# Kernel tuning notes

Measured on AMD Instinct MI355X. Metric: run time of the kernel, lower is better.

## Reference

```python
import jax, jax.numpy as jnp
import numpy as np

N_NODES = 20000
N_EDGES = 320000
N_GRAPHS = 64
D = 128  # node_dim


def _gat_conv(h, W, al, ar, b, src, dst, n, res=None, act=None):
    # DGL GATConv: fc -> per-head attn logits -> leaky_relu -> edge softmax per dst -> scatter-add
    H, Dh = al.shape
    feat = (h @ W).reshape(n, H, Dh)                      # [N,H,D]
    el = jnp.einsum('nhd,hd->nh', feat, al)               # [N,H]
    er = jnp.einsum('nhd,hd->nh', feat, ar)               # [N,H]
    e = jax.nn.leaky_relu(el[src] + er[dst], 0.2)         # [E,H]
    m = jax.ops.segment_max(e, dst, num_segments=n)       # [N,H]
    m = jnp.where(jnp.isfinite(m), m, 0.0)
    a = jnp.exp(e - m[dst])                               # [E,H]
    den = jax.ops.segment_sum(a, dst, num_segments=n)     # [N,H]
    a = a / jnp.maximum(den, 1e-9)[dst]
    out = jax.ops.segment_sum(a[:, :, None] * feat[src], dst, num_segments=n)  # [N,H,D]
    if res is not None:
        out = out + res
    out = out + b.reshape(1, H, Dh)
    return act(out) if act is not None else out


def setup_inputs() -> dict:
    key = jax.random.key(0)
    ks = jax.random.split(key, 20)
    s = 0.05
    inp = {
        'h': jax.random.normal(ks[0], (N_NODES, D), jnp.float32),
        'he': jax.random.normal(ks[1], (N_EDGES, 64), jnp.float32),
        'src': jax.random.randint(ks[2], (N_EDGES,), 0, N_NODES),
        'dst': jax.random.randint(ks[3], (N_EDGES,), 0, N_NODES),
        'graph_id': jnp.sort(jax.random.randint(ks[4], (N_NODES,), 0, N_GRAPHS)),
        # layer 0: in=D, heads=4, out=D
        'W0': jax.random.normal(ks[5], (D, 4 * D), jnp.float32) * s,
        'al0': jax.random.normal(ks[6], (4, D), jnp.float32) * s,
        'ar0': jax.random.normal(ks[7], (4, D), jnp.float32) * s,
        'b0': jnp.zeros((4 * D,), jnp.float32),
        # layer 1: in=4D, heads=4, out=D, residual (identity since 4D==4*D)
        'W1': jax.random.normal(ks[8], (4 * D, 4 * D), jnp.float32) * s,
        'al1': jax.random.normal(ks[9], (4, D), jnp.float32) * s,
        'ar1': jax.random.normal(ks[10], (4, D), jnp.float32) * s,
        'b1': jnp.zeros((4 * D,), jnp.float32),
        # layer 2: in=4D, heads=6, out=D, residual via res_fc (4D -> 6D)
        'W2': jax.random.normal(ks[11], (4 * D, 6 * D), jnp.float32) * s,
        'al2': jax.random.normal(ks[12], (6, D), jnp.float32) * s,
        'ar2': jax.random.normal(ks[13], (6, D), jnp.float32) * s,
        'b2': jnp.zeros((6 * D,), jnp.float32),
        'resW2': jax.random.normal(ks[14], (4 * D, 6 * D), jnp.float32) * s,
        # final MLP (1 layer): Linear(D, D)
        'Wm': jax.random.normal(ks[15], (D, D), jnp.float32) * s,
        'bm': jnp.zeros((D,), jnp.float32),
    }
    return inp


def reference(h, he, src, dst, graph_id, W0, al0, ar0, b0, W1, al1, ar1, b1,
              W2, al2, ar2, b2, resW2, Wm, bm):
    n = h.shape[0]
    elu = jax.nn.elu
    # layer 0 (no residual, elu), flatten heads
    x = _gat_conv(h, W0, al0, ar0, b0, src, dst, n, res=None, act=elu)
    x = x.reshape(n, -1)  # [N, 4D]
    # layer 1 (identity residual, elu), flatten heads
    res1 = x.reshape(n, 4, D)
    x2 = _gat_conv(x, W1, al1, ar1, b1, src, dst, n, res=res1, act=elu)
    x2 = x2.reshape(n, -1)  # [N, 4D]
    # layer 2 (linear residual, no activation), mean over heads
    res2 = (x2 @ resW2).reshape(n, 6, D)
    x3 = _gat_conv(x2, W2, al2, ar2, b2, src, dst, n, res=res2, act=None)
    local_feat = x3.mean(axis=1)  # [N, D]
    # avg pooling per graph + linear
    sums = jax.ops.segment_sum(local_feat, graph_id, num_segments=N_GRAPHS)
    cnts = jax.ops.segment_sum(jnp.ones((n,), local_feat.dtype), graph_id, num_segments=N_GRAPHS)
    pooled = sums / jnp.maximum(cnts, 1.0)[:, None]  # [G, D]
    global_feat = pooled @ Wm + bm
    return (local_feat, global_feat)
```

## Files before the change

### kernel.cpp

```cpp
#include <hip/hip_runtime.h>
#include <math.h>


typedef _Float16 f16;
typedef __attribute__((ext_vector_type(8))) _Float16 half8;
typedef __attribute__((ext_vector_type(4))) _Float16 half4;
typedef __attribute__((ext_vector_type(4))) float float4v;

union U16 { unsigned short u; _Float16 h; };

#define M_PAD 20096
#define CHSTRIDE ((size_t)M_PAD * 64)

__device__ inline void gload_lds16(const void* g, void* l) {
    __builtin_amdgcn_global_load_lds((const __attribute__((address_space(1))) unsigned*)g,
                                     (__attribute__((address_space(3))) unsigned*)l,
                                     16, 0, 0);
}


__global__ __launch_bounds__(256) void deg_kernel(const int* __restrict__ dst,
                                                  int* __restrict__ deg, int E) {
    int e = blockIdx.x * 256 + threadIdx.x;
    if (e < E) atomicAdd(&deg[dst[e]], 1);
}

__global__ __launch_bounds__(1024) void scan_kernel(const int* __restrict__ deg,
                                                    int* __restrict__ row_off,
                                                    const int* __restrict__ gid,
                                                    int* __restrict__ gstart, int n) {
    __shared__ int sums[1024];
    int t = threadIdx.x;
    if (t <= 64) {
        int g = t, lo = 0, hi = n;
        while (lo < hi) {
            int mid = (lo + hi) >> 1;
            if (gid[mid] < g) lo = mid + 1; else hi = mid;
        }
        gstart[g] = lo;
    }
    int CH = (n + 1023) >> 10;
    int base = t * CH;
    int s = 0;
    for (int i = 0; i < CH; ++i) { int idx = base + i; if (idx < n) s += deg[idx]; }
    sums[t] = s;
    __syncthreads();
    for (int off = 1; off < 1024; off <<= 1) {
        int v = (t >= off) ? sums[t - off] : 0;
        __syncthreads();
        sums[t] += v;
        __syncthreads();
    }
    int run = (t == 0) ? 0 : sums[t - 1];
    for (int i = 0; i < CH; ++i) {
        int idx = base + i;
        if (idx < n) { row_off[idx] = run; run += deg[idx]; }
    }
    if (t == 1023) row_off[n] = run;
}

__global__ __launch_bounds__(256) void fill_kernel(const int* __restrict__ src,
                                                   const int* __restrict__ dst,
                                                   const int* __restrict__ row_off,
                                                   int* __restrict__ fill,
                                                   int* __restrict__ csr_src, int E) {
    int e = blockIdx.x * 256 + threadIdx.x;
    if (e < E) {
        int d = dst[e];
        int pos = row_off[d] + atomicAdd(&fill[d], 1);
        csr_src[pos] = src[e];
    }
}


__global__ __launch_bounds__(256) void prep_kernel(
        const float* __restrict__ h, f16* __restrict__ h16,
        f16* __restrict__ x1, f16* __restrict__ x2,
        const float* __restrict__ W0, f16* __restrict__ Wt0,
        const float* __restrict__ W1, f16* __restrict__ Wt1,
        const float* __restrict__ W2, const float* __restrict__ resW2,
        f16* __restrict__ Wt2cat,
        int* __restrict__ deg2, int n) {
    __shared__ float tile[32][33];
    int b = blockIdx.x;
    int t = threadIdx.x;
    if (b < 2512) {
        long i = ((long)b * 256 + t) * 4;
        long nv = (long)n * 128;
        float4 v = make_float4(0.f, 0.f, 0.f, 0.f);
        if (i < nv) v = *(const float4*)&h[i];
        half4 o; o[0] = (f16)v.x; o[1] = (f16)v.y; o[2] = (f16)v.z; o[3] = (f16)v.w;
        *(half4*)&h16[i] = o;
        return;
    }
    b -= 2512;
    if (b < 48) {
        int idx = (b * 256 + t) * 4;
        int total = (M_PAD - n) * 512;
        if (idx < total) {
            half4 z; z[0] = (f16)0.f; z[1] = (f16)0.f; z[2] = (f16)0.f; z[3] = (f16)0.f;
            *(half4*)&x1[(size_t)n * 512 + idx] = z;
            *(half4*)&x2[(size_t)n * 512 + idx] = z;
        }
        return;
    }
    b -= 48;
    {
        const float* W = nullptr; f16* Wt = nullptr;
        int K = 0, N = 0, bx = 0, by = 0;
        bool dotr = false;
        if (b < 64)        { W = W0; Wt = Wt0;    K = 128; N = 512; bx = b & 15;  by = b >> 4; dotr = true; }
        else if (b < 320)  { int r = b - 64;  W = W1; Wt = Wt1;    K = 512; N = 512; bx = r & 15;  by = r >> 4; dotr = true; }
        else if (b < 704)  { int r = b - 320; W = W2; Wt = Wt2cat; K = 512; N = 768; bx = r % 24;  by = r / 24; dotr = true; }
        if (dotr) {
            int tx = t & 31, ty = t >> 5;
            int n0 = bx * 32, k0 = by * 32;
#pragma unroll
            for (int i = 0; i < 32; i += 8)
                tile[ty + i][tx] = W[(size_t)(k0 + ty + i) * N + n0 + tx];
            __syncthreads();
#pragma unroll
            for (int i = 0; i < 32; i += 8)
                Wt[(size_t)(n0 + ty + i) * K + k0 + tx] = (f16)tile[tx][ty + i];
            return;
        }
    }
    b -= 704;
    if (b < 256) {
        int idx = b * 256 + t;
        int d = idx >> 9;
        int k = idx & 511;
        float s = 0.f;
#pragma unroll
        for (int hh = 0; hh < 6; ++hh) s += resW2[(size_t)k * 768 + hh * 128 + d];
        Wt2cat[(size_t)(768 + d) * 512 + k] = (f16)(s * (1.f / 6.f));
        return;
    }
    b -= 256;
    {
        int idx = (b * 256 + t) * 4;
        if (idx < 2 * n) *(int4*)&deg2[idx] = make_int4(0, 0, 0, 0);
    }
}


#define STAGE(buf, k0) do {                                   \
    f16* a_ = As + (buf) * 2048 + t * 8;                      \
    f16* b_ = Bs + (buf) * 4096 + t * 8;                      \
    gload_lds16(ag0 + (k0), a_);                              \
    gload_lds16(bg0 + (k0), b_);                              \
    gload_lds16(bg1 + (k0), b_ + 2048);                       \
} while (0)

__global__ __launch_bounds__(256) void gemm16_kernel(const f16* __restrict__ A,
                                                     const f16* __restrict__ Bt,
                                                     f16* __restrict__ Cc,
                                                     f16* __restrict__ Cr,
                                                     const float* __restrict__ al,
                                                     const float* __restrict__ ar,
                                                     float* __restrict__ el8,
                                                     float* __restrict__ er8,
                                                     int N, int K, int nchunk,
                                                     int nheads, int nvalid) {
    __shared__ f16 As[2 * 64 * 32];
    __shared__ f16 Bs[2 * 128 * 32];
    __shared__ float elds[2][2][64];
    int t = threadIdx.x;
    int w = t >> 6;
    int l = t & 63;

    int gx = gridDim.x;
    int nwg = gx * gridDim.y;
    int wg = blockIdx.y * gx + blockIdx.x;
    int qq = nwg >> 3, rr = nwg & 7;
    int xcd = wg & 7, idx = wg >> 3;
    int swz = (xcd < rr ? xcd * (qq + 1) : rr * (qq + 1) + (xcd - rr) * qq) + idx;
    int bxi = swz % gx;
    int byi = swz / gx;

    size_t bm = (size_t)byi * 64;
    int bn = bxi * 128;
    int wm = (w & 1) * 32;
    int wn = (w >> 1) * 64;

    int srow = t >> 2;
    int sq = (t & 3) ^ ((srow >> 1) & 3);
    const f16* ag0 = A + (bm + srow) * K + sq * 8;
    const f16* bg0 = Bt + (size_t)(bn + srow) * K + sq * 8;
    const f16* bg1 = Bt + (size_t)(bn + 64 + srow) * K + sq * 8;

    float4v acc[2][4];
#pragma unroll
    for (int i = 0; i < 2; ++i)
#pragma unroll
        for (int j = 0; j < 4; ++j) acc[i][j] = (float4v)(0.f);

    int ml = l & 15, q = l >> 4;
    int sslot = (q ^ ((ml >> 1) & 3)) * 8;
    int apoff = (wm + ml) * 32 + sslot;
    int bpoff = (wn + ml) * 32 + sslot;

    STAGE(0, 0);
    __syncthreads();
    int cur = 0;
    for (int k0 = 0; k0 < K; k0 += 32) {
        if (k0 + 32 < K) STAGE(cur ^ 1, k0 + 32);
        const f16* ap = As + cur * 2048 + apoff;
        const f16* bp = Bs + cur * 4096 + bpoff;
        half8 af[2], bf[4];
#pragma unroll
        for (int mt = 0; mt < 2; ++mt) af[mt] = *(const half8*)(ap + mt * 16 * 32);
#pragma unroll
        for (int nt = 0; nt < 4; ++nt) bf[nt] = *(const half8*)(bp + nt * 16 * 32);
#pragma unroll
        for (int mt = 0; mt < 2; ++mt)
#pragma unroll
            for (int nt = 0; nt < 4; ++nt)
                acc[mt][nt] = __builtin_amdgcn_mfma_f32_16x16x32_f16(bf[nt], af[mt],
                                                                     acc[mt][nt], 0, 0, 0);
        __syncthreads();
        cur ^= 1;
    }
#pragma unroll
    for (int mt = 0; mt < 2; ++mt) {
        size_t row = bm + wm + mt * 16 + ml;
#pragma unroll
        for (int nt = 0; nt < 4; ++nt) {
            half4 hv;
#pragma unroll
            for (int r = 0; r < 4; ++r) hv[r] = (f16)acc[mt][nt][r];
            int col = bn + wn + nt * 16 + q * 4;
            if (col < nchunk) {
                *(half4*)&Cc[(size_t)(col >> 6) * CHSTRIDE + row * 64 + (col & 63)] = hv;
            } else {
                *(half4*)&Cr[row * (size_t)(N - nchunk) + (col - nchunk)] = hv;
            }
        }
    }
    if (al != nullptr && bn < nheads * 128) {
        int hh = bn >> 7;
        float4 a4[4], r4[4];
#pragma unroll
        for (int nt = 0; nt < 4; ++nt) {
            int ci = hh * 128 + wn + nt * 16 + q * 4;
            a4[nt] = *(const float4*)&al[ci];
            r4[nt] = *(const float4*)&ar[ci];
        }
        int wnidx = wn >> 6;
#pragma unroll
        for (int mt = 0; mt < 2; ++mt) {
            float ep = 0.f, rp = 0.f;
#pragma unroll
            for (int nt = 0; nt < 4; ++nt) {
                ep += acc[mt][nt][0] * a4[nt].x + acc[mt][nt][1] * a4[nt].y
                    + acc[mt][nt][2] * a4[nt].z + acc[mt][nt][3] * a4[nt].w;
                rp += acc[mt][nt][0] * r4[nt].x + acc[mt][nt][1] * r4[nt].y
                    + acc[mt][nt][2] * r4[nt].z + acc[mt][nt][3] * r4[nt].w;
            }
            ep += __shfl_xor(ep, 16, 64); ep += __shfl_xor(ep, 32, 64);
            rp += __shfl_xor(rp, 16, 64); rp += __shfl_xor(rp, 32, 64);
            if (q == 0) {
                elds[0][wnidx][wm + mt * 16 + ml] = ep;
                elds[1][wnidx][wm + mt * 16 + ml] = rp;
            }
        }
        __syncthreads();
        if (((t >> 6) & 1) == 0) {
            int row = t & 63, which = t >> 7;
            long gv = (long)bm + row;
            if (gv < nvalid) {
                float vs = elds[which][0][row] + elds[which][1][row];
                if (which == 0) el8[gv * 8 + hh] = vs;
                else            er8[gv * 8 + hh] = vs;
            }
        }
    }
}


__global__ __launch_bounds__(256, 8) void edge_weight_kernel(
        const float* __restrict__ el8, const float* __restrict__ er8,
        const int* __restrict__ row_off, const int* __restrict__ csr_src,
        int* __restrict__ wp, float* __restrict__ inv8,
        int H, int n, int E) {
    int wid = threadIdx.x >> 6, lane = threadIdx.x & 63;
    int c2 = lane >> 4;
    int sl = lane & 15;
    int v = blockIdx.x * 16 + wid * 4 + c2;
    if (v >= n) return;
    float era[6];
    {
        float4 a = *(const float4*)&er8[(size_t)v * 8];
        float2 b = *(const float2*)&er8[(size_t)v * 8 + 4];
        era[0] = a.x; era[1] = a.y; era[2] = a.z; era[3] = a.w;
        era[4] = b.x; era[5] = b.y;
    }
    int beg = row_off[v], end = row_off[v + 1];
    float lsum[6] = {0.f, 0.f, 0.f, 0.f, 0.f, 0.f};
    for (int pos = beg; pos < end; pos += 16) {
        int cnt = min(16, end - pos);
        int s_l = (sl < cnt) ? csr_src[pos + sl] : 0;
        float4 a = *(const float4*)&el8[(size_t)s_l * 8];
        float2 bq = *(const float2*)&el8[(size_t)s_l * 8 + 4];
        float ee[6] = {a.x, a.y, a.z, a.w, bq.x, bq.y};
#pragma unroll
        for (int h = 0; h < 6; ++h) {
            if (h < H) {
                float lg = ee[h] + era[h];
                lg = (lg >= 0.f) ? lg : 0.2f * lg;
                float wv = __expf(lg);
                if (sl >= cnt) wv = 0.f;
                lsum[h] += wv;
                if (sl < cnt) {
                    U16 uu; uu.h = (f16)wv;
                    wp[(size_t)h * E + pos + sl] = s_l | ((int)uu.u << 16);
                }
            }
        }
    }
#pragma unroll
    for (int h = 0; h < 6; ++h)
#pragma unroll
        for (int off = 8; off >= 1; off >>= 1)
            lsum[h] += __shfl_xor(lsum[h], off, 64);
    if (sl == 0) {
#pragma unroll
        for (int h = 0; h < 6; ++h)
            if (h < H) inv8[(size_t)v * 8 + h] = 1.f / fmaxf(lsum[h], 1e-9f);
    }
}


__device__ __forceinline__ void agg_chunk_body(
        const f16* __restrict__ fc, const int* __restrict__ wp,
        const float* __restrict__ inv8, int head,
        const int* __restrict__ row_off,
        const f16* __restrict__ res, const float* __restrict__ bias,
        f16* __restrict__ out16, float* __restrict__ out32,
        int n, int width, int act, int chunk,
        int wave_id, int wavestride, int lane) {
    int c = lane >> 3;
    int j = lane & 7;
    int coff = j * 8;
    int cb = chunk * 64 + coff;
    float4 bv0 = *(const float4*)&bias[cb];
    float4 bv1 = *(const float4*)&bias[cb + 4];
    int clbase = lane & 56;

    for (int v0 = wave_id * 8; v0 < n; v0 += wavestride * 8) {
        int v = v0 + c;
        bool valid = (v < n);
        int beg = 0, end = 0;
        if (valid) { beg = row_off[v]; end = row_off[v + 1]; }
        int rounds = end - beg;
        rounds = max(rounds, __shfl_xor(rounds, 8, 64));
        rounds = max(rounds, __shfl_xor(rounds, 16, 64));
        rounds = max(rounds, __shfl_xor(rounds, 32, 64));
        float acc[8] = {0.f, 0.f, 0.f, 0.f, 0.f, 0.f, 0.f, 0.f};
        int pidx = beg + j;
        int pk = (pidx < end) ? wp[pidx] : 0;
        for (int base = 0; base < rounds; base += 8) {
            int pn = beg + base + 8 + j;
            int pk_nxt = (pn < end) ? wp[pn] : 0;
#pragma unroll
            for (int hg = 0; hg < 2; ++hg) {
                int cb4 = clbase + hg * 4;
                int p0 = __shfl(pk, cb4 + 0, 64);
                int p1 = __shfl(pk, cb4 + 1, 64);
                int p2 = __shfl(pk, cb4 + 2, 64);
                int p3 = __shfl(pk, cb4 + 3, 64);
                half8 f0 = *(const half8*)&fc[(size_t)(p0 & 0xFFFF) * 64 + coff];
                half8 f1 = *(const half8*)&fc[(size_t)(p1 & 0xFFFF) * 64 + coff];
                half8 f2 = *(const half8*)&fc[(size_t)(p2 & 0xFFFF) * 64 + coff];
                half8 f3 = *(const half8*)&fc[(size_t)(p3 & 0xFFFF) * 64 + coff];
                U16 u0; u0.u = (unsigned short)((unsigned)p0 >> 16); float w0 = (float)u0.h;
                U16 u1; u1.u = (unsigned short)((unsigned)p1 >> 16); float w1 = (float)u1.h;
                U16 u2; u2.u = (unsigned short)((unsigned)p2 >> 16); float w2 = (float)u2.h;
                U16 u3; u3.u = (unsigned short)((unsigned)p3 >> 16); float w3 = (float)u3.h;
#pragma unroll
                for (int k = 0; k < 8; ++k) acc[k] += w0 * (float)f0[k];
#pragma unroll
                for (int k = 0; k < 8; ++k) acc[k] += w1 * (float)f1[k];
#pragma unroll
                for (int k = 0; k < 8; ++k) acc[k] += w2 * (float)f2[k];
#pragma unroll
                for (int k = 0; k < 8; ++k) acc[k] += w3 * (float)f3[k];
            }
            pk = pk_nxt;
        }
        if (valid) {
            float inv = inv8[(size_t)v * 8 + head];
            float ox[8];
#pragma unroll
            for (int k = 0; k < 8; ++k) ox[k] = acc[k] * inv;
            size_t base = (size_t)v * width + cb;
            if (res) {
                half8 rr = *(const half8*)&res[base];
#pragma unroll
                for (int k = 0; k < 8; ++k) ox[k] += (float)rr[k];
            }
            ox[0] += bv0.x; ox[1] += bv0.y; ox[2] += bv0.z; ox[3] += bv0.w;
            ox[4] += bv1.x; ox[5] += bv1.y; ox[6] += bv1.z; ox[7] += bv1.w;
            if (act) {
#pragma unroll
                for (int k = 0; k < 8; ++k)
                    ox[k] = (ox[k] > 0.f) ? ox[k] : expm1f(ox[k]);
            }
            if (out16) {
                half8 o;
#pragma unroll
                for (int k = 0; k < 8; ++k) o[k] = (f16)ox[k];
                *(half8*)&out16[base] = o;
            } else {
                *(float4*)&out32[base]     = make_float4(ox[0], ox[1], ox[2], ox[3]);
                *(float4*)&out32[base + 4] = make_float4(ox[4], ox[5], ox[6], ox[7]);
            }
        }
    }
}

__global__ __launch_bounds__(256, 6) void agg_chunk_kernel(
        const f16* __restrict__ featc, const int* __restrict__ wp,
        const float* __restrict__ inv8,
        const int* __restrict__ row_off,
        const f16* __restrict__ res, const float* __restrict__ bias,
        f16* __restrict__ out16, float* __restrict__ out32,
        int n, int nchunks, int width, int E, int act) {
    int wid = threadIdx.x >> 6, lane = threadIdx.x & 63;
    int b = blockIdx.x;
    {
        int chunk = b & 7;
        agg_chunk_body(featc + (size_t)chunk * CHSTRIDE, wp + (size_t)(chunk >> 1) * E,
                       inv8, chunk >> 1, row_off, res, bias, out16, out32,
                       n, width, act, chunk, (b >> 3) * 4 + wid, 1024, lane);
    }
    if (nchunks > 8) {
        int chunk = 8 + (b & 3);
        if (chunk < nchunks)
            agg_chunk_body(featc + (size_t)chunk * CHSTRIDE, wp + (size_t)(chunk >> 1) * E,
                           inv8, chunk >> 1, row_off, res, bias, out16, out32,
                           n, width, act, chunk, (b >> 2) * 4 + wid, 2048, lane);
    }
}


__global__ __launch_bounds__(128) void mean_pool_kernel(const f16* __restrict__ x3,
                                                        const f16* __restrict__ resm,
                                                        float* __restrict__ local, int n) {
    int v = blockIdx.x;
    int d = threadIdx.x;
    const f16* p = x3 + (size_t)v * 768;
    float s = 0.f;
#pragma unroll
    for (int h = 0; h < 6; ++h) s += (float)p[h * 128 + d];
    local[(size_t)v * 128 + d] = s * (1.f / 6.f) + (float)resm[(size_t)v * 128 + d];
}


__global__ __launch_bounds__(1024) void graph_pool_kernel(const float* __restrict__ local,
                                                          const int* __restrict__ gstart,
                                                          const float* __restrict__ Wm,
                                                          const float* __restrict__ bm,
                                                          float* __restrict__ gout) {
    __shared__ float buf[8][128];
    __shared__ float p[128];
    int g = blockIdx.x;
    int t = threadIdx.x;
    int c = t & 127;
    int sub = t >> 7;
    int beg = gstart[g], end = gstart[g + 1];
    float s = 0.f;
    for (int v = beg + sub; v < end; v += 8) s += local[(size_t)v * 128 + c];
    buf[sub][c] = s;
    __syncthreads();
    if (sub == 0) {
        float tot = 0.f;
#pragma unroll
        for (int k = 0; k < 8; ++k) tot += buf[k][c];
        float cntf = fmaxf((float)(end - beg), 1.f);
        p[c] = tot / cntf;
    }
    __syncthreads();
    if (t < 128) {
        float s2 = 0.f;
#pragma unroll 16
        for (int k = 0; k < 128; ++k) s2 += p[k] * Wm[k * 128 + t];
        gout[g * 128 + t] = s2 + bm[t];
    }
}


extern "C" void kernel_launch(void* const* d_in, const int* in_sizes, int n_in,
                              void* d_out, int out_size, void* d_ws, size_t ws_size,
                              hipStream_t stream) {
    const float* h     = (const float*)d_in[0];
    const int*   src   = (const int*)d_in[2];
    const int*   dst   = (const int*)d_in[3];
    const int*   gid   = (const int*)d_in[4];
    const float* W0    = (const float*)d_in[5];
    const float* al0   = (const float*)d_in[6];
    const float* ar0   = (const float*)d_in[7];
    const float* b0    = (const float*)d_in[8];
    const float* W1    = (const float*)d_in[9];
    const float* al1   = (const float*)d_in[10];
    const float* ar1   = (const float*)d_in[11];
    const float* b1    = (const float*)d_in[12];
    const float* W2    = (const float*)d_in[13];
    const float* al2   = (const float*)d_in[14];
    const float* ar2   = (const float*)d_in[15];
    const float* b2    = (const float*)d_in[16];
    const float* resW2 = (const float*)d_in[17];
    const float* Wm    = (const float*)d_in[18];
    const float* bm    = (const float*)d_in[19];

    const int n = in_sizes[0] / 128;
    const int E = in_sizes[2];

    size_t off = 0;
    auto take = [&](size_t bytes) -> void* {
        void* p = (char*)d_ws + off;
        off = (off + bytes + 255) & ~(size_t)255;
        return p;
    };
    f16* h16     = (f16*)take((size_t)M_PAD * 128 * 2);
    f16* Wt0     = (f16*)take((size_t)512 * 128 * 2);
    f16* Wt1     = (f16*)take((size_t)512 * 512 * 2);
    f16* Wt2cat  = (f16*)take((size_t)896 * 512 * 2);
    f16* featc   = (f16*)take((size_t)12 * CHSTRIDE * 2);
    f16* resm    = (f16*)take((size_t)M_PAD * 128 * 2);
    f16* x1_16   = (f16*)take((size_t)M_PAD * 512 * 2);
    f16* x2_16   = (f16*)take((size_t)M_PAD * 512 * 2);
    f16* x3h     = (f16*)take((size_t)n * 768 * 2);
    int* wp      = (int*)take((size_t)6 * E * 4);
    float* inv8  = (float*)take((size_t)n * 8 * 4);
    float* el8   = (float*)take((size_t)n * 8 * 4);
    float* er8   = (float*)take((size_t)n * 8 * 4);
    int* deg     = (int*)take((size_t)2 * n * 4);
    int* fillc   = deg + n;
    int* row_off = (int*)take((size_t)(n + 1) * 4);
    int* csr_src = (int*)take((size_t)E * 4);
    int* gstart  = (int*)take(65 * 4);

    float* out_local  = (float*)d_out;
    float* out_global = (float*)d_out + (size_t)n * 128;

    prep_kernel<<<3560, 256, 0, stream>>>(h, h16, x1_16, x2_16, W0, Wt0, W1, Wt1,
                                          W2, resW2, Wt2cat, deg, n);

    deg_kernel<<<(E + 255) / 256, 256, 0, stream>>>(dst, deg, E);
    scan_kernel<<<1, 1024, 0, stream>>>(deg, row_off, gid, gstart, n);
    fill_kernel<<<(E + 255) / 256, 256, 0, stream>>>(src, dst, row_off, fillc, csr_src, E);

    const int gy = M_PAD / 64;
    const int ew_blocks = (n + 15) / 16;

    gemm16_kernel<<<dim3(512 / 128, gy), 256, 0, stream>>>(h16, Wt0, featc, nullptr,
                                                           al0, ar0, el8, er8, 512, 128, 512, 4, n);
    edge_weight_kernel<<<ew_blocks, 256, 0, stream>>>(el8, er8, row_off, csr_src, wp, inv8, 4, n, E);
    agg_chunk_kernel<<<2048, 256, 0, stream>>>(featc, wp, inv8, row_off,
                                               nullptr, b0, x1_16, nullptr, n, 8, 512, E, 1);
    gemm16_kernel<<<dim3(512 / 128, gy), 256, 0, stream>>>(x1_16, Wt1, featc, nullptr,
                                                           al1, ar1, el8, er8, 512, 512, 512, 4, n);
    edge_weight_kernel<<<ew_blocks, 256, 0, stream>>>(el8, er8, row_off, csr_src, wp, inv8, 4, n, E);
    agg_chunk_kernel<<<2048, 256, 0, stream>>>(featc, wp, inv8, row_off,
                                               x1_16, b1, x2_16, nullptr, n, 8, 512, E, 1);
    gemm16_kernel<<<dim3(896 / 128, gy), 256, 0, stream>>>(x2_16, Wt2cat, featc, resm,
                                                           al2, ar2, el8, er8, 896, 512, 768, 6, n);
    edge_weight_kernel<<<ew_blocks, 256, 0, stream>>>(el8, er8, row_off, csr_src, wp, inv8, 6, n, E);
    agg_chunk_kernel<<<2048, 256, 0, stream>>>(featc, wp, inv8, row_off,
                                               nullptr, b2, x3h, nullptr, n, 12, 768, E, 0);
    mean_pool_kernel<<<n, 128, 0, stream>>>(x3h, resm, out_local, n);
    graph_pool_kernel<<<64, 1024, 0, stream>>>(out_local, gstart, Wm, bm, out_global);
}
```

Baseline: 498.0 us.

## Sort destination nodes by in-degree to balance warp work in edge kernels

Builds a degree-bucketed permutation of nodes inside the scan kernel using a shared-memory histogram and counting sort. The edge-weight and aggregation kernels then process nodes in permuted order, so the nodes grouped into one wave have similar degrees and the max-degree round count wastes fewer lanes. This adds an indirection load per node and scatters output writes and feature reads across memory, which may reduce locality. The single-block scan kernel also gets extra serial work.

```diff
diff --git a/kernel.cpp b/kernel.cpp
--- a/kernel.cpp
+++ b/kernel.cpp
@@ -28,8 +28,10 @@
 __global__ __launch_bounds__(1024) void scan_kernel(const int* __restrict__ deg,
                                                     int* __restrict__ row_off,
                                                     const int* __restrict__ gid,
-                                                    int* __restrict__ gstart, int n) {
+                                                    int* __restrict__ gstart,
+                                                    int* __restrict__ perm, int n) {
     __shared__ int sums[1024];
+    __shared__ int hist[256];
     int t = threadIdx.x;
     if (t <= 64) {
         int g = t, lo = 0, hi = n;
@@ -57,6 +59,29 @@
         if (idx < n) { row_off[idx] = run; run += deg[idx]; }
     }
     if (t == 1023) row_off[n] = run;
+
+    if (t < 256) hist[t] = 0;
+    __syncthreads();
+    for (int i = 0; i < CH; ++i) {
+        int idx = base + i;
+        if (idx < n) atomicAdd(&hist[min(deg[idx], 255)], 1);
+    }
+    __syncthreads();
+    int excl = 0;
+    if (t < 256) {
+        for (int k = 0; k < t; ++k) excl += hist[k];
+    }
+    __syncthreads();
+    if (t < 256) hist[t] = excl;
+    __syncthreads();
+    for (int i = 0; i < CH; ++i) {
+        int idx = base + i;
+        if (idx < n) {
+            int d = min(deg[idx], 255);
+            int pos = atomicAdd(&hist[d], 1);
+            perm[pos] = idx;
+        }
+    }
 }
 
 __global__ __launch_bounds__(256) void fill_kernel(const int* __restrict__ src,
@@ -281,6 +306,7 @@
 __global__ __launch_bounds__(256, 8) void edge_weight_kernel(
         const float* __restrict__ el8, const float* __restrict__ er8,
         const int* __restrict__ row_off, const int* __restrict__ csr_src,
+        const int* __restrict__ perm,
         int* __restrict__ wp, float* __restrict__ inv8,
         int H, int n, int E) {
     int wid = threadIdx.x >> 6, lane = threadIdx.x & 63;
@@ -288,6 +314,7 @@
     int sl = lane & 15;
     int v = blockIdx.x * 16 + wid * 4 + c2;
     if (v >= n) return;
+    v = perm[v];
     float era[6];
     {
         float4 a = *(const float4*)&er8[(size_t)v * 8];
@@ -334,7 +361,7 @@
 __device__ __forceinline__ void agg_chunk_body(
         const f16* __restrict__ fc, const int* __restrict__ wp,
         const float* __restrict__ inv8, int head,
-        const int* __restrict__ row_off,
+        const int* __restrict__ row_off, const int* __restrict__ perm,
         const f16* __restrict__ res, const float* __restrict__ bias,
         f16* __restrict__ out16, float* __restrict__ out32,
         int n, int width, int act, int chunk,
@@ -348,8 +375,9 @@
     int clbase = lane & 56;
 
     for (int v0 = wave_id * 8; v0 < n; v0 += wavestride * 8) {
-        int v = v0 + c;
-        bool valid = (v < n);
+        int vi = v0 + c;
+        bool valid = (vi < n);
+        int v = valid ? perm[vi] : 0;
         int beg = 0, end = 0;
         if (valid) { beg = row_off[v]; end = row_off[v + 1]; }
         int rounds = end - beg;
@@ -422,7 +450,7 @@
 __global__ __launch_bounds__(256, 6) void agg_chunk_kernel(
         const f16* __restrict__ featc, const int* __restrict__ wp,
         const float* __restrict__ inv8,
-        const int* __restrict__ row_off,
+        const int* __restrict__ row_off, const int* __restrict__ perm,
         const f16* __restrict__ res, const float* __restrict__ bias,
         f16* __restrict__ out16, float* __restrict__ out32,
         int n, int nchunks, int width, int E, int act) {
@@ -431,14 +459,14 @@
     {
         int chunk = b & 7;
         agg_chunk_body(featc + (size_t)chunk * CHSTRIDE, wp + (size_t)(chunk >> 1) * E,
-                       inv8, chunk >> 1, row_off, res, bias, out16, out32,
+                       inv8, chunk >> 1, row_off, perm, res, bias, out16, out32,
                        n, width, act, chunk, (b >> 3) * 4 + wid, 1024, lane);
     }
     if (nchunks > 8) {
         int chunk = 8 + (b & 3);
         if (chunk < nchunks)
             agg_chunk_body(featc + (size_t)chunk * CHSTRIDE, wp + (size_t)(chunk >> 1) * E,
-                           inv8, chunk >> 1, row_off, res, bias, out16, out32,
+                           inv8, chunk >> 1, row_off, perm, res, bias, out16, out32,
                            n, width, act, chunk, (b >> 2) * 4 + wid, 2048, lane);
     }
 }
@@ -539,6 +567,7 @@
     int* fillc   = deg + n;
     int* row_off = (int*)take((size_t)(n + 1) * 4);
     int* csr_src = (int*)take((size_t)E * 4);
+    int* perm    = (int*)take((size_t)n * 4);
     int* gstart  = (int*)take(65 * 4);
 
     float* out_local  = (float*)d_out;
@@ -548,7 +577,7 @@
                                           W2, resW2, Wt2cat, deg, n);
 
     deg_kernel<<<(E + 255) / 256, 256, 0, stream>>>(dst, deg, E);
-    scan_kernel<<<1, 1024, 0, stream>>>(deg, row_off, gid, gstart, n);
+    scan_kernel<<<1, 1024, 0, stream>>>(deg, row_off, gid, gstart, perm, n);
     fill_kernel<<<(E + 255) / 256, 256, 0, stream>>>(src, dst, row_off, fillc, csr_src, E);
 
     const int gy = M_PAD / 64;
@@ -556,18 +585,18 @@
 
     gemm16_kernel<<<dim3(512 / 128, gy), 256, 0, stream>>>(h16, Wt0, featc, nullptr,
                                                            al0, ar0, el8, er8, 512, 128, 512, 4, n);
-    edge_weight_kernel<<<ew_blocks, 256, 0, stream>>>(el8, er8, row_off, csr_src, wp, inv8, 4, n, E);
-    agg_chunk_kernel<<<2048, 256, 0, stream>>>(featc, wp, inv8, row_off,
+    edge_weight_kernel<<<ew_blocks, 256, 0, stream>>>(el8, er8, row_off, csr_src, perm, wp, inv8, 4, n, E);
+    agg_chunk_kernel<<<2048, 256, 0, stream>>>(featc, wp, inv8, row_off, perm,
                                                nullptr, b0, x1_16, nullptr, n, 8, 512, E, 1);
     gemm16_kernel<<<dim3(512 / 128, gy), 256, 0, stream>>>(x1_16, Wt1, featc, nullptr,
                                                            al1, ar1, el8, er8, 512, 512, 512, 4, n);
-    edge_weight_kernel<<<ew_blocks, 256, 0, stream>>>(el8, er8, row_off, csr_src, wp, inv8, 4, n, E);
-    agg_chunk_kernel<<<2048, 256, 0, stream>>>(featc, wp, inv8, row_off,
+    edge_weight_kernel<<<ew_blocks, 256, 0, stream>>>(el8, er8, row_off, csr_src, perm, wp, inv8, 4, n, E);
+    agg_chunk_kernel<<<2048, 256, 0, stream>>>(featc, wp, inv8, row_off, perm,
                                                x1_16, b1, x2_16, nullptr, n, 8, 512, E, 1);
     gemm16_kernel<<<dim3(896 / 128, gy), 256, 0, stream>>>(x2_16, Wt2cat, featc, resm,
                                                            al2, ar2, el8, er8, 896, 512, 768, 6, n);
-    edge_weight_kernel<<<ew_blocks, 256, 0, stream>>>(el8, er8, row_off, csr_src, wp, inv8, 6, n, E);
-    agg_chunk_kernel<<<2048, 256, 0, stream>>>(featc, wp, inv8, row_off,
+    edge_weight_kernel<<<ew_blocks, 256, 0, stream>>>(el8, er8, row_off, csr_src, perm, wp, inv8, 6, n, E);
+    agg_chunk_kernel<<<2048, 256, 0, stream>>>(featc, wp, inv8, row_off, perm,
                                                nullptr, b2, x3h, nullptr, n, 12, 768, E, 0);
     mean_pool_kernel<<<n, 128, 0, stream>>>(x3h, resm, out_local, n);
     graph_pool_kernel<<<64, 1024, 0, stream>>>(out_local, gstart, Wm, bm, out_global);
```

New measurement: 518.2 us. 4.1% more time.
